# Optimization experiments

Hardware: AMD Instinct MI355X
Metric: run time of the kernel (lower is better)

## Reference

```python
import jax, jax.numpy as jnp
import numpy as np

B, N, E, H = 8, 16, 256, 256
EPS = 1e-5


def _ln(x, g, b):
    m = jnp.mean(x, axis=-1, keepdims=True)
    v = jnp.mean(jnp.square(x - m), axis=-1, keepdims=True)
    return (x - m) * jax.lax.rsqrt(v + EPS) * g + b


def setup_inputs() -> dict:
    key = jax.random.key(0)
    ks = jax.random.split(key, 24)
    s = 0.05
    inp = {
        "source_entities": jax.random.normal(ks[0], (B, N, E), jnp.float32),
        "source_relations": jax.random.uniform(ks[1], (B, N, N), jnp.float32),
        "target_entities": jax.random.normal(ks[2], (B, N, E), jnp.float32),
        "target_relations": jax.random.uniform(ks[3], (B, N, N), jnp.float32),
        # relation_encoder: Linear(2E->H), LayerNorm(H), ReLU, Linear(H->H)
        "rel_W1": jax.random.normal(ks[4], (2 * E, H), jnp.float32) * s,
        "rel_b1": jnp.zeros((H,), jnp.float32),
        "rel_g1": jnp.ones((H,), jnp.float32),
        "rel_be1": jnp.zeros((H,), jnp.float32),
        "rel_W2": jax.random.normal(ks[5], (H, H), jnp.float32) * s,
        "rel_b2": jnp.zeros((H,), jnp.float32),
        # mapping_network: Linear(2H->H), LayerNorm(H), ReLU, Linear(H->1)
        "map_W1": jax.random.normal(ks[6], (2 * H, H), jnp.float32) * s,
        "map_b1": jnp.zeros((H,), jnp.float32),
        "map_g": jnp.ones((H,), jnp.float32),
        "map_be": jnp.zeros((H,), jnp.float32),
        "map_W2": jax.random.normal(ks[7], (H, 1), jnp.float32) * s,
        "map_b2": jnp.zeros((1,), jnp.float32),
        # correspondence_scorer: Linear(2E->H), ReLU, Linear(H->1)
        "cor_W1": jax.random.normal(ks[8], (2 * E, H), jnp.float32) * s,
        "cor_b1": jnp.zeros((H,), jnp.float32),
        "cor_W2": jax.random.normal(ks[9], (H, 1), jnp.float32) * s,
        "cor_b2": jnp.zeros((1,), jnp.float32),
    }
    return inp


def _encode_relations(ent, rel, W1, b1, g1, be1, W2, b2):
    # ent: [B,N,E]; rel: [B,N,N].  Equivalent to cat([e_i, e_j]) @ W1 by
    # splitting W1 into the rows multiplying e_i and e_j (avoids concat).
    Wi, Wj = W1[:E], W1[E:]
    h = (jnp.einsum("bie,eh->bih", ent, Wi)[:, :, None, :]
         + jnp.einsum("bje,eh->bjh", ent, Wj)[:, None, :, :] + b1)  # [B,N,N,H]
    h = jax.nn.relu(_ln(h, g1, be1))
    h = jnp.einsum("bijh,hk->bijk", h, W2) + b2
    mask = (rel > 0).astype(h.dtype)[..., None]
    h = h * mask  # zeros where no relation, matching scatter into zeros tensor
    return h.reshape(ent.shape[0], N * N, H)


def _pairwise_score(a, b, W1, b1, W2, b2, g=None, be=None):
    # score over all (i,j) pairs: cat([a_i, b_j]) -> MLP -> scalar
    d = a.shape[-1]
    Wa, Wb = W1[:d], W1[d:]
    h = (jnp.einsum("bsd,dh->bsh", a, Wa)[:, :, None, :]
         + jnp.einsum("btd,dh->bth", b, Wb)[:, None, :, :] + b1)  # [B,S,T,H]
    if g is not None:
        h = _ln(h, g, be)
    h = jax.nn.relu(h)
    return (jnp.einsum("bsth,ho->bsto", h, W2) + b2)[..., 0]  # [B,S,T]


def reference(source_entities, source_relations, target_entities, target_relations,
              rel_W1, rel_b1, rel_g1, rel_be1, rel_W2, rel_b2,
              map_W1, map_b1, map_g, map_be, map_W2, map_b2,
              cor_W1, cor_b1, cor_W2, cor_b2):
    src_rel = _encode_relations(source_entities, source_relations,
                                rel_W1, rel_b1, rel_g1, rel_be1, rel_W2, rel_b2)
    tgt_rel = _encode_relations(target_entities, target_relations,
                                rel_W1, rel_b1, rel_g1, rel_be1, rel_W2, rel_b2)
    mapping_scores = _pairwise_score(src_rel, tgt_rel, map_W1, map_b1,
                                     map_W2, map_b2, map_g, map_be)
    corr_scores = _pairwise_score(source_entities, target_entities,
                                  cor_W1, cor_b1, cor_W2, cor_b2)
    mapping_scores = jax.nn.softmax(mapping_scores, axis=-1)
    corr_scores = jax.nn.softmax(corr_scores, axis=-1)
    return mapping_scores, corr_scores
```

## Files before the change

### kernel.cpp

```cpp
#include <hip/hip_runtime.h>

#define EDIM 256
#define HDIM 256

typedef float v2f __attribute__((ext_vector_type(2)));
__device__ __forceinline__ v2f splat2(float x) { v2f r; r.x = x; r.y = x; return r; }
__device__ __forceinline__ v2f mk2(float a, float b) { v2f r; r.x = a; r.y = b; return r; }
__device__ __forceinline__ v2f pkfma(v2f a, v2f b, v2f c) { return __builtin_elementwise_fma(a, b, c); }

__device__ __forceinline__ float waveAllSum(float v) {
  #pragma unroll
  for (int m = 32; m >= 1; m >>= 1) v += __shfl_xor(v, m, 64);
  return v;
}

__global__ __launch_bounds__(256) void k_proj(
    const float* __restrict__ srcE, const float* __restrict__ tgtE,
    const float* __restrict__ relW1, const float* __restrict__ relb1,
    const float* __restrict__ corW1, const float* __restrict__ corb1,
    const float* __restrict__ relW2, const float* __restrict__ relb2,
    const float* __restrict__ mapW1,
    float* __restrict__ Ps, float* __restrict__ Qs,
    float* __restrict__ Pt, float* __restrict__ Qt,
    float* __restrict__ CA, float* __restrict__ CB,
    float* __restrict__ Ca, float* __restrict__ Cb,
    float* __restrict__ da, float* __restrict__ db)
{
  const int which = blockIdx.x & 7;
  const int xb    = blockIdx.x >> 3;
  const int h     = threadIdx.x;
  if (which < 6 && xb >= 16) return;
  const int row0  = xb * 8;

  const float* A = nullptr; const float* W; const float* bias = nullptr;
  float* out;
  if (which == 0)      { A = srcE; W = relW1;              bias = relb1; out = Ps; }
  else if (which == 1) { A = srcE; W = relW1 + EDIM*HDIM;  out = Qs; }
  else if (which == 2) { A = tgtE; W = relW1;              bias = relb1; out = Pt; }
  else if (which == 3) { A = tgtE; W = relW1 + EDIM*HDIM;  out = Qt; }
  else if (which == 4) { A = srcE; W = corW1;              out = CA; }
  else if (which == 5) { A = tgtE; W = corW1 + EDIM*HDIM;  bias = corb1; out = CB; }
  else if (which == 6) { W = mapW1;                        out = Ca; }
  else                 { W = mapW1 + EDIM*HDIM;            out = Cb; }

  __shared__ float arow[8][EDIM];
  if (which < 6) {
    #pragma unroll
    for (int r = 0; r < 8; ++r) arow[r][h] = A[(row0 + r)*EDIM + h];
  } else if (xb < 32) {
    #pragma unroll
    for (int r = 0; r < 8; ++r) arow[r][h] = relW2[(row0 + r)*EDIM + h];
  } else {
    #pragma unroll
    for (int r = 0; r < 8; ++r) arow[r][h] = relb2[h];
  }
  __syncthreads();

  float acc[8];
  const float init = bias ? bias[h] : 0.0f;
  #pragma unroll
  for (int r = 0; r < 8; ++r) acc[r] = init;

  for (int d = 0; d < EDIM; d += 4) {
    const float w0 = W[(d+0)*HDIM + h];
    const float w1 = W[(d+1)*HDIM + h];
    const float w2 = W[(d+2)*HDIM + h];
    const float w3 = W[(d+3)*HDIM + h];
    #pragma unroll
    for (int r = 0; r < 8; ++r) {
      const float4 av = *(const float4*)&arow[r][d];
      acc[r] = fmaf(av.x,w0, fmaf(av.y,w1, fmaf(av.z,w2, fmaf(av.w,w3, acc[r]))));
    }
  }

  if (which < 6 || xb < 32) {
    #pragma unroll
    for (int r = 0; r < 8; ++r) out[(row0 + r)*HDIM + h] = acc[r];
  } else {
    float* d = (which == 6) ? da : db;
    d[h] = acc[0];
  }
}

__global__ __launch_bounds__(512) void k_encode(
    const float* __restrict__ Ps, const float* __restrict__ Qs,
    const float* __restrict__ relS,
    const float* __restrict__ Pt, const float* __restrict__ Qt,
    const float* __restrict__ relT,
    const float* __restrict__ g1, const float* __restrict__ be1,
    const float* __restrict__ Ca, const float* __restrict__ Cb,
    const float* __restrict__ da, const float* __restrict__ db,
    const float* __restrict__ mapb1,
    const float* __restrict__ mapg, const float* __restrict__ mapbe,
    const float* __restrict__ mapW2,
    float2* __restrict__ SAp, float* __restrict__ SAr, float* __restrict__ TB,
    float* __restrict__ rsS, float* __restrict__ qsS,
    float* __restrict__ rsT, float* __restrict__ qsT,
    float4* __restrict__ gbw)
{
  const int side = blockIdx.x & 1;
  const int bx   = blockIdx.x >> 1;
  const float* P   = side ? Pt   : Ps;
  const float* Q   = side ? Qt   : Qs;
  const float* rel = side ? relT : relS;

  const int row0 = bx * 8;
  const int b   = row0 >> 8;
  const int ij0 = row0 & 255;
  const int i   = ij0 >> 4;
  const int j0  = ij0 & 15;
  const int tid  = threadIdx.x;
  const int h    = tid & 255;
  const int rg   = tid >> 8;
  const int wave = tid >> 6;
  const int lane = tid & 63;

  if (side == 0 && bx == 0 && rg == 0)
    gbw[h] = make_float4(mapg[h], mapbe[h], mapW2[h], 0.0f);

  __shared__ v2f rlp[2][2][HDIM];
  __shared__ float red[8][8];

  const float pv = P[(b*16 + i)*HDIM + h];
  float x[4];
  #pragma unroll
  for (int r = 0; r < 4; ++r) x[r] = pv + Q[(b*16 + j0 + rg*4 + r)*HDIM + h];

  {
    float s1[4], s2[4];
    #pragma unroll
    for (int r = 0; r < 4; ++r) { s1[r] = x[r]; s2[r] = x[r]*x[r]; }
    #pragma unroll
    for (int m = 32; m >= 1; m >>= 1) {
      #pragma unroll
      for (int r = 0; r < 4; ++r) {
        s1[r] += __shfl_xor(s1[r], m, 64);
        s2[r] += __shfl_xor(s2[r], m, 64);
      }
    }
    if (lane == 0) {
      #pragma unroll
      for (int r = 0; r < 4; ++r) { red[wave][2*r] = s1[r]; red[wave][2*r+1] = s2[r]; }
    }
  }
  __syncthreads();

  {
    const float gh = g1[h], beh = be1[h];
    const int wb = rg*4;
    float val[4];
    #pragma unroll
    for (int r = 0; r < 4; ++r) {
      const float S1 = red[wb+0][2*r] + red[wb+1][2*r] + red[wb+2][2*r] + red[wb+3][2*r];
      const float S2 = red[wb+0][2*r+1] + red[wb+1][2*r+1] + red[wb+2][2*r+1] + red[wb+3][2*r+1];
      const float mean = S1 * (1.0f/256.0f);
      const float var  = S2 * (1.0f/256.0f) - mean*mean;
      const float rinv = rsqrtf(var + 1e-5f);
      val[r] = fmaxf(fmaf((x[r] - mean)*rinv, gh, beh), 0.0f);
    }
    rlp[rg][0][h] = mk2(val[0], val[1]);
    rlp[rg][1][h] = mk2(val[2], val[3]);
  }
  __syncthreads();

  const float* C = side ? Cb : Ca;
  v2f c01 = {0.f,0.f}, c23 = {0.f,0.f};
  #pragma unroll 2
  for (int k = 0; k < HDIM; k += 4) {
    const float w0 = C[(k+0)*HDIM + h];
    const float w1 = C[(k+1)*HDIM + h];
    const float w2 = C[(k+2)*HDIM + h];
    const float w3 = C[(k+3)*HDIM + h];
    const float4 pa = *(const float4*)&rlp[rg][0][k];
    const float4 pb = *(const float4*)&rlp[rg][0][k+2];
    const float4 qa = *(const float4*)&rlp[rg][1][k];
    const float4 qb = *(const float4*)&rlp[rg][1][k+2];
    c01 = pkfma(mk2(pa.x,pa.y), splat2(w0), c01);
    c01 = pkfma(mk2(pa.z,pa.w), splat2(w1), c01);
    c01 = pkfma(mk2(pb.x,pb.y), splat2(w2), c01);
    c01 = pkfma(mk2(pb.z,pb.w), splat2(w3), c01);
    c23 = pkfma(mk2(qa.x,qa.y), splat2(w0), c23);
    c23 = pkfma(mk2(qa.z,qa.w), splat2(w1), c23);
    c23 = pkfma(mk2(qb.x,qb.y), splat2(w2), c23);
    c23 = pkfma(mk2(qb.z,qb.w), splat2(w3), c23);
  }

  {
    const float dv = (side ? db : da)[h];
    c01 = c01 + splat2(dv);
    c23 = c23 + splat2(dv);
    const float* relRow = rel + (b*16 + i)*16;
    const int jb = j0 + rg*4;
    const v2f m01 = mk2(relRow[jb+0] > 0.f ? 1.f : 0.f, relRow[jb+1] > 0.f ? 1.f : 0.f);
    const v2f m23 = mk2(relRow[jb+2] > 0.f ? 1.f : 0.f, relRow[jb+3] > 0.f ? 1.f : 0.f);
    c01 = c01 * m01;
    c23 = c23 * m23;
    if (side) {
      const float mb = mapb1[h];
      c01 = c01 + splat2(mb);
      c23 = c23 + splat2(mb);
    }
  }

  {
    float s1[4] = {c01.x, c01.y, c23.x, c23.y};
    float s2[4] = {c01.x*c01.x, c01.y*c01.y, c23.x*c23.x, c23.y*c23.y};
    #pragma unroll
    for (int m = 32; m >= 1; m >>= 1) {
      #pragma unroll
      for (int r = 0; r < 4; ++r) {
        s1[r] += __shfl_xor(s1[r], m, 64);
        s2[r] += __shfl_xor(s2[r], m, 64);
      }
    }
    __syncthreads();
    if (lane == 0) {
      #pragma unroll
      for (int r = 0; r < 4; ++r) { red[wave][2*r] = s1[r]; red[wave][2*r+1] = s2[r]; }
    }
  }
  __syncthreads();
  if (tid < 16) {
    const int rg2 = tid >> 3, idx = tid & 7, r = idx >> 1;
    const int wb = rg2*4;
    const float v = red[wb+0][idx] + red[wb+1][idx] + red[wb+2][idx] + red[wb+3][idx];
    float* rs = side ? rsT : rsS;
    float* qs = side ? qsT : qsS;
    const int row = row0 + rg2*4 + r;
    if (idx & 1) qs[row] = v; else rs[row] = v;
  }

  const int rbase = row0 + rg*4;
  if (side == 0) {
    const int spBase = b*128 + ((ij0 + rg*4) >> 1);
    SAp[(spBase + 0)*HDIM + h] = make_float2(c01.x, c01.y);
    SAp[(spBase + 1)*HDIM + h] = make_float2(c23.x, c23.y);
    SAr[(rbase + 0)*HDIM + h] = c01.x;
    SAr[(rbase + 1)*HDIM + h] = c01.y;
    SAr[(rbase + 2)*HDIM + h] = c23.x;
    SAr[(rbase + 3)*HDIM + h] = c23.y;
  } else {
    TB[(rbase + 0)*HDIM + h] = c01.x;
    TB[(rbase + 1)*HDIM + h] = c01.y;
    TB[(rbase + 2)*HDIM + h] = c23.x;
    TB[(rbase + 3)*HDIM + h] = c23.y;
  }
}

__global__ __launch_bounds__(256) void k_cross(
    const float* __restrict__ SAr, const float* __restrict__ TB,
    float* __restrict__ G)
{
  const int b    = blockIdx.x & 7;
  const int rest = blockIdx.x >> 3;
  const int s0 = (rest & 7) * 32;
  const int t0 = (rest >> 3) * 32;
  const int tx = threadIdx.x & 15;
  const int ty = threadIdx.x >> 4;

  const float* SAb = SAr + ((b<<8) + s0)*HDIM;
  const float* TBb = TB  + ((b<<8) + t0)*HDIM;

  __shared__ float As[32][68], Bs[32][68];
  float acc00 = 0.f, acc01 = 0.f, acc10 = 0.f, acc11 = 0.f;

  const int lr = threadIdx.x >> 3;
  const int lc = (threadIdx.x & 7) * 8;

  for (int kk = 0; kk < HDIM; kk += 64) {
    *(float4*)&As[lr][lc]   = *(const float4*)&SAb[lr*HDIM + kk + lc];
    *(float4*)&As[lr][lc+4] = *(const float4*)&SAb[lr*HDIM + kk + lc + 4];
    *(float4*)&Bs[lr][lc]   = *(const float4*)&TBb[lr*HDIM + kk + lc];
    *(float4*)&Bs[lr][lc+4] = *(const float4*)&TBb[lr*HDIM + kk + lc + 4];
    __syncthreads();
    #pragma unroll
    for (int k = 0; k < 64; k += 4) {
      const float4 a0 = *(const float4*)&As[tx][k];
      const float4 a1 = *(const float4*)&As[tx+16][k];
      const float4 b0 = *(const float4*)&Bs[ty][k];
      const float4 b1 = *(const float4*)&Bs[ty+16][k];
      acc00 = fmaf(a0.x,b0.x, fmaf(a0.y,b0.y, fmaf(a0.z,b0.z, fmaf(a0.w,b0.w, acc00))));
      acc01 = fmaf(a0.x,b1.x, fmaf(a0.y,b1.y, fmaf(a0.z,b1.z, fmaf(a0.w,b1.w, acc01))));
      acc10 = fmaf(a1.x,b0.x, fmaf(a1.y,b0.y, fmaf(a1.z,b0.z, fmaf(a1.w,b0.w, acc10))));
      acc11 = fmaf(a1.x,b1.x, fmaf(a1.y,b1.y, fmaf(a1.z,b1.z, fmaf(a1.w,b1.w, acc11))));
    }
    __syncthreads();
  }

  float* Gb = G + (((b<<8) + t0)<<8) + s0;
  Gb[(ty   )*256 + tx     ] = acc00;
  Gb[(ty   )*256 + tx + 16] = acc10;
  Gb[(ty+16)*256 + tx     ] = acc01;
  Gb[(ty+16)*256 + tx + 16] = acc11;
}

__global__ __launch_bounds__(256) void k_scores(
    const float2* __restrict__ SApf, const float* __restrict__ TB,
    const float* __restrict__ G,
    const float* __restrict__ rsS, const float* __restrict__ qsS,
    const float* __restrict__ rsT, const float* __restrict__ qsT,
    const float4* __restrict__ gbw,
    const float* __restrict__ CA, const float* __restrict__ CB,
    const float* __restrict__ cW2,
    float* __restrict__ mapOut, float* __restrict__ corOut)
{
  const int wave = threadIdx.x >> 6;
  const int lane = threadIdx.x & 63;

  if (blockIdx.x >= 512) {
    const int bs = (blockIdx.x - 512)*4 + wave;
    const int b  = bs >> 4;
    const float4 ca4 = *(const float4*)(CA + bs*HDIM + lane*4);
    const float4 w24 = *(const float4*)(cW2 + lane*4);
    float sc[16];
    #pragma unroll
    for (int t = 0; t < 16; ++t) {
      const float4 cb4 = *(const float4*)(CB + (b*16 + t)*HDIM + lane*4);
      float p = fmaxf(ca4.x + cb4.x, 0.0f)*w24.x
              + fmaxf(ca4.y + cb4.y, 0.0f)*w24.y
              + fmaxf(ca4.z + cb4.z, 0.0f)*w24.z
              + fmaxf(ca4.w + cb4.w, 0.0f)*w24.w;
      sc[t] = waveAllSum(p);
    }
    float mx = sc[0];
    #pragma unroll
    for (int t = 1; t < 16; ++t) mx = fmaxf(mx, sc[t]);
    float se = 0.0f;
    #pragma unroll
    for (int t = 0; t < 16; ++t) { sc[t] = __expf(sc[t] - mx); se += sc[t]; }
    if (lane < 16) corOut[bs*16 + lane] = sc[lane] / se;
    return;
  }

  const int b  = blockIdx.x & 7;
  const int s0 = (blockIdx.x >> 3) * 4;
  const int t  = (wave << 6) + lane;

  const float* tbrow = TB + ((b<<8) + t)*HDIM;
  const v2f* sp0 = (const v2f*)SApf + ((b<<7) + (s0>>1))*HDIM;
  const v2f* sp1 = sp0 + HDIM;

  v2f al01, bt01, al23, bt23;
  {
    const float4 gv = *(const float4*)&G[(((b<<8) + t)<<8) + s0];
    const float rt = rsT[(b<<8) + t];
    const float qt = qsT[(b<<8) + t];
    const float Gv[4] = {gv.x, gv.y, gv.z, gv.w};
    float alv[4], btv[4];
    #pragma unroll
    for (int si = 0; si < 4; ++si) {
      const float mean = (rsS[(b<<8) + s0 + si] + rt) * (1.0f/256.0f);
      const float e2   = (qsS[(b<<8) + s0 + si] + qt + 2.0f*Gv[si]) * (1.0f/256.0f);
      const float rinv = rsqrtf(e2 - mean*mean + 1e-5f);
      alv[si] = rinv;
      btv[si] = -mean * rinv;
    }
    al01 = mk2(alv[0], alv[1]); bt01 = mk2(btv[0], btv[1]);
    al23 = mk2(alv[2], alv[3]); bt23 = mk2(btv[2], btv[3]);
  }

  v2f acc01 = {0.f,0.f}, acc23 = {0.f,0.f};
  const v2f zero = {0.f,0.f};
  #pragma unroll 2
  for (int h = 0; h < HDIM; h += 4) {
    const float4 tb4 = *(const float4*)&tbrow[h];
    const v2f a0 = sp0[h], a1 = sp0[h+1], a2 = sp0[h+2], a3 = sp0[h+3];
    const v2f c0 = sp1[h], c1 = sp1[h+1], c2 = sp1[h+2], c3 = sp1[h+3];
    const float4 q0 = gbw[h], q1 = gbw[h+1], q2 = gbw[h+2], q3 = gbw[h+3];
    v2f u, r;
    u = pkfma(a0 + splat2(tb4.x), al01, bt01);
    r = __builtin_elementwise_max(pkfma(u, splat2(q0.x), splat2(q0.y)), zero);
    acc01 = pkfma(r, splat2(q0.z), acc01);
    u = pkfma(c0 + splat2(tb4.x), al23, bt23);
    r = __builtin_elementwise_max(pkfma(u, splat2(q0.x), splat2(q0.y)), zero);
    acc23 = pkfma(r, splat2(q0.z), acc23);

    u = pkfma(a1 + splat2(tb4.y), al01, bt01);
    r = __builtin_elementwise_max(pkfma(u, splat2(q1.x), splat2(q1.y)), zero);
    acc01 = pkfma(r, splat2(q1.z), acc01);
    u = pkfma(c1 + splat2(tb4.y), al23, bt23);
    r = __builtin_elementwise_max(pkfma(u, splat2(q1.x), splat2(q1.y)), zero);
    acc23 = pkfma(r, splat2(q1.z), acc23);

    u = pkfma(a2 + splat2(tb4.z), al01, bt01);
    r = __builtin_elementwise_max(pkfma(u, splat2(q2.x), splat2(q2.y)), zero);
    acc01 = pkfma(r, splat2(q2.z), acc01);
    u = pkfma(c2 + splat2(tb4.z), al23, bt23);
    r = __builtin_elementwise_max(pkfma(u, splat2(q2.x), splat2(q2.y)), zero);
    acc23 = pkfma(r, splat2(q2.z), acc23);

    u = pkfma(a3 + splat2(tb4.w), al01, bt01);
    r = __builtin_elementwise_max(pkfma(u, splat2(q3.x), splat2(q3.y)), zero);
    acc01 = pkfma(r, splat2(q3.z), acc01);
    u = pkfma(c3 + splat2(tb4.w), al23, bt23);
    r = __builtin_elementwise_max(pkfma(u, splat2(q3.x), splat2(q3.y)), zero);
    acc23 = pkfma(r, splat2(q3.z), acc23);
  }

  __shared__ float sc[4][256];
  sc[0][t] = acc01.x; sc[1][t] = acc01.y; sc[2][t] = acc23.x; sc[3][t] = acc23.y;
  __syncthreads();

  float v0 = sc[wave][lane];
  float v1 = sc[wave][lane + 64];
  float v2 = sc[wave][lane + 128];
  float v3 = sc[wave][lane + 192];
  float mx = fmaxf(fmaxf(v0, v1), fmaxf(v2, v3));
  #pragma unroll
  for (int m = 32; m >= 1; m >>= 1) mx = fmaxf(mx, __shfl_xor(mx, m, 64));
  const float e0 = __expf(v0 - mx), e1 = __expf(v1 - mx);
  const float e2 = __expf(v2 - mx), e3 = __expf(v3 - mx);
  const float se = waveAllSum(e0 + e1 + e2 + e3);
  const float inv = 1.0f / se;
  float* orow = mapOut + ((b<<8) + s0 + wave)*256;
  orow[lane]       = e0 * inv;
  orow[lane + 64]  = e1 * inv;
  orow[lane + 128] = e2 * inv;
  orow[lane + 192] = e3 * inv;
}

extern "C" void kernel_launch(void* const* d_in, const int* in_sizes, int n_in,
                              void* d_out, int out_size, void* d_ws, size_t ws_size,
                              hipStream_t stream) {
  const float* srcE  = (const float*)d_in[0];
  const float* srcR  = (const float*)d_in[1];
  const float* tgtE  = (const float*)d_in[2];
  const float* tgtR  = (const float*)d_in[3];
  const float* relW1 = (const float*)d_in[4];
  const float* relb1 = (const float*)d_in[5];
  const float* relg1 = (const float*)d_in[6];
  const float* relbe1= (const float*)d_in[7];
  const float* relW2 = (const float*)d_in[8];
  const float* relb2 = (const float*)d_in[9];
  const float* mapW1 = (const float*)d_in[10];
  const float* mapb1 = (const float*)d_in[11];
  const float* mapg  = (const float*)d_in[12];
  const float* mapbe = (const float*)d_in[13];
  const float* mapW2 = (const float*)d_in[14];
  const float* corW1 = (const float*)d_in[16];
  const float* corb1 = (const float*)d_in[17];
  const float* corW2 = (const float*)d_in[18];

  float* ws   = (float*)d_ws;
  float* Ps   = ws;
  float* Qs   = Ps   + 32768;
  float* Pt   = Qs   + 32768;
  float* Qt   = Pt   + 32768;
  float* CA   = Qt   + 32768;
  float* CB   = CA   + 32768;
  float2* SAp = (float2*)(CB + 32768);
  float* SAr  = (float*)(SAp + 262144);
  float* TB   = SAr + 524288;
  float* G    = TB  + 524288;
  float* rsS  = G + 524288;
  float* qsS  = rsS + 2048;
  float* rsT  = qsS + 2048;
  float* qsT  = rsT + 2048;
  float4* gbw = (float4*)(qsT + 2048);
  float* Ca   = (float*)gbw + 1024;
  float* Cb   = Ca + 65536;
  float* da   = Cb + 65536;
  float* db   = da + 256;

  float* mapOut = (float*)d_out;
  float* corOut = mapOut + 524288;

  k_proj<<<264, 256, 0, stream>>>(srcE, tgtE, relW1, relb1, corW1, corb1,
                                  relW2, relb2, mapW1,
                                  Ps, Qs, Pt, Qt, CA, CB,
                                  Ca, Cb, da, db);
  k_encode<<<512, 512, 0, stream>>>(Ps, Qs, srcR,
                                    Pt, Qt, tgtR,
                                    relg1, relbe1,
                                    Ca, Cb, da, db,
                                    mapb1, mapg, mapbe, mapW2,
                                    SAp, SAr, TB, rsS, qsS, rsT, qsT, gbw);
  k_cross<<<512, 256, 0, stream>>>(SAr, TB, G);
  k_scores<<<544, 256, 0, stream>>>(SAp, TB, G, rsS, qsS, rsT, qsT, gbw,
                                    CA, CB, corW2, mapOut, corOut);
}
```

Baseline: 68.60 us.

## Split k_scores hidden dim across waves and compute eight source rows per block

```diff
diff --git a/kernel.cpp b/kernel.cpp
--- a/kernel.cpp
+++ b/kernel.cpp
@@ -294,7 +294,7 @@
   Gb[(ty+16)*256 + tx + 16] = acc11;
 }
 
-__global__ __launch_bounds__(256) void k_scores(
+__global__ __launch_bounds__(1024) void k_scores(
     const float2* __restrict__ SApf, const float* __restrict__ TB,
     const float* __restrict__ G,
     const float* __restrict__ rsS, const float* __restrict__ qsS,
@@ -307,8 +307,8 @@
   const int wave = threadIdx.x >> 6;
   const int lane = threadIdx.x & 63;
 
-  if (blockIdx.x >= 512) {
-    const int bs = (blockIdx.x - 512)*4 + wave;
+  if (blockIdx.x >= 256) {
+    const int bs = (blockIdx.x - 256)*16 + wave;
     const int b  = bs >> 4;
     const float4 ca4 = *(const float4*)(CA + bs*HDIM + lane*4);
     const float4 w24 = *(const float4*)(cW2 + lane*4);
@@ -333,90 +333,101 @@
   }
 
   const int b  = blockIdx.x & 7;
-  const int s0 = (blockIdx.x >> 3) * 4;
-  const int t  = (wave << 6) + lane;
+  const int s0 = (blockIdx.x >> 3) * 8;
+  const int tq = wave & 3;
+  const int hq = wave >> 2;
+  const int t  = (tq << 6) + lane;
+  const int h0 = __builtin_amdgcn_readfirstlane(hq * 64);
 
   const float* tbrow = TB + ((b<<8) + t)*HDIM;
-  const v2f* sp0 = (const v2f*)SApf + ((b<<7) + (s0>>1))*HDIM;
-  const v2f* sp1 = sp0 + HDIM;
-
-  v2f al01, bt01, al23, bt23;
+  const v2f* sp[4];
+  #pragma unroll
+  for (int p = 0; p < 4; ++p)
+    sp[p] = (const v2f*)SApf + ((b<<7) + (s0>>1) + p)*HDIM;
+
+  v2f al[4], bt[4];
   {
-    const float4 gv = *(const float4*)&G[(((b<<8) + t)<<8) + s0];
+    const float4 gv0 = *(const float4*)&G[(((b<<8) + t)<<8) + s0];
+    const float4 gv1 = *(const float4*)&G[(((b<<8) + t)<<8) + s0 + 4];
     const float rt = rsT[(b<<8) + t];
     const float qt = qsT[(b<<8) + t];
-    const float Gv[4] = {gv.x, gv.y, gv.z, gv.w};
-    float alv[4], btv[4];
-    #pragma unroll
-    for (int si = 0; si < 4; ++si) {
+    const float Gv[8] = {gv0.x, gv0.y, gv0.z, gv0.w, gv1.x, gv1.y, gv1.z, gv1.w};
+    float alv[8], btv[8];
+    #pragma unroll
+    for (int si = 0; si < 8; ++si) {
       const float mean = (rsS[(b<<8) + s0 + si] + rt) * (1.0f/256.0f);
       const float e2   = (qsS[(b<<8) + s0 + si] + qt + 2.0f*Gv[si]) * (1.0f/256.0f);
       const float rinv = rsqrtf(e2 - mean*mean + 1e-5f);
       alv[si] = rinv;
       btv[si] = -mean * rinv;
     }
-    al01 = mk2(alv[0], alv[1]); bt01 = mk2(btv[0], btv[1]);
-    al23 = mk2(alv[2], alv[3]); bt23 = mk2(btv[2], btv[3]);
-  }
-
-  v2f acc01 = {0.f,0.f}, acc23 = {0.f,0.f};
+    #pragma unroll
+    for (int p = 0; p < 4; ++p) {
+      al[p] = mk2(alv[2*p], alv[2*p+1]);
+      bt[p] = mk2(btv[2*p], btv[2*p+1]);
+    }
+  }
+
+  v2f acc[4] = {{0.f,0.f},{0.f,0.f},{0.f,0.f},{0.f,0.f}};
   const v2f zero = {0.f,0.f};
   #pragma unroll 2
-  for (int h = 0; h < HDIM; h += 4) {
+  for (int h = h0; h < h0 + 64; h += 4) {
     const float4 tb4 = *(const float4*)&tbrow[h];
-    const v2f a0 = sp0[h], a1 = sp0[h+1], a2 = sp0[h+2], a3 = sp0[h+3];
-    const v2f c0 = sp1[h], c1 = sp1[h+1], c2 = sp1[h+2], c3 = sp1[h+3];
     const float4 q0 = gbw[h], q1 = gbw[h+1], q2 = gbw[h+2], q3 = gbw[h+3];
-    v2f u, r;
-    u = pkfma(a0 + splat2(tb4.x), al01, bt01);
-    r = __builtin_elementwise_max(pkfma(u, splat2(q0.x), splat2(q0.y)), zero);
-    acc01 = pkfma(r, splat2(q0.z), acc01);
-    u = pkfma(c0 + splat2(tb4.x), al23, bt23);
-    r = __builtin_elementwise_max(pkfma(u, splat2(q0.x), splat2(q0.y)), zero);
-    acc23 = pkfma(r, splat2(q0.z), acc23);
-
-    u = pkfma(a1 + splat2(tb4.y), al01, bt01);
-    r = __builtin_elementwise_max(pkfma(u, splat2(q1.x), splat2(q1.y)), zero);
-    acc01 = pkfma(r, splat2(q1.z), acc01);
-    u = pkfma(c1 + splat2(tb4.y), al23, bt23);
-    r = __builtin_elementwise_max(pkfma(u, splat2(q1.x), splat2(q1.y)), zero);
-    acc23 = pkfma(r, splat2(q1.z), acc23);
-
-    u = pkfma(a2 + splat2(tb4.z), al01, bt01);
-    r = __builtin_elementwise_max(pkfma(u, splat2(q2.x), splat2(q2.y)), zero);
-    acc01 = pkfma(r, splat2(q2.z), acc01);
-    u = pkfma(c2 + splat2(tb4.z), al23, bt23);
-    r = __builtin_elementwise_max(pkfma(u, splat2(q2.x), splat2(q2.y)), zero);
-    acc23 = pkfma(r, splat2(q2.z), acc23);
-
-    u = pkfma(a3 + splat2(tb4.w), al01, bt01);
-    r = __builtin_elementwise_max(pkfma(u, splat2(q3.x), splat2(q3.y)), zero);
-    acc01 = pkfma(r, splat2(q3.z), acc01);
-    u = pkfma(c3 + splat2(tb4.w), al23, bt23);
-    r = __builtin_elementwise_max(pkfma(u, splat2(q3.x), splat2(q3.y)), zero);
-    acc23 = pkfma(r, splat2(q3.z), acc23);
-  }
-
-  __shared__ float sc[4][256];
-  sc[0][t] = acc01.x; sc[1][t] = acc01.y; sc[2][t] = acc23.x; sc[3][t] = acc23.y;
-  __syncthreads();
-
-  float v0 = sc[wave][lane];
-  float v1 = sc[wave][lane + 64];
-  float v2 = sc[wave][lane + 128];
-  float v3 = sc[wave][lane + 192];
-  float mx = fmaxf(fmaxf(v0, v1), fmaxf(v2, v3));
+    #pragma unroll
+    for (int p = 0; p < 4; ++p) {
+      const v2f a0 = sp[p][h], a1 = sp[p][h+1], a2 = sp[p][h+2], a3 = sp[p][h+3];
+      v2f u, r;
+      u = pkfma(a0 + splat2(tb4.x), al[p], bt[p]);
+      r = __builtin_elementwise_max(pkfma(u, splat2(q0.x), splat2(q0.y)), zero);
+      acc[p] = pkfma(r, splat2(q0.z), acc[p]);
+      u = pkfma(a1 + splat2(tb4.y), al[p], bt[p]);
+      r = __builtin_elementwise_max(pkfma(u, splat2(q1.x), splat2(q1.y)), zero);
+      acc[p] = pkfma(r, splat2(q1.z), acc[p]);
+      u = pkfma(a2 + splat2(tb4.z), al[p], bt[p]);
+      r = __builtin_elementwise_max(pkfma(u, splat2(q2.x), splat2(q2.y)), zero);
+      acc[p] = pkfma(r, splat2(q2.z), acc[p]);
+      u = pkfma(a3 + splat2(tb4.w), al[p], bt[p]);
+      r = __builtin_elementwise_max(pkfma(u, splat2(q3.x), splat2(q3.y)), zero);
+      acc[p] = pkfma(r, splat2(q3.z), acc[p]);
+    }
+  }
+
+  __shared__ float pg[4][4][8][64];
   #pragma unroll
-  for (int m = 32; m >= 1; m >>= 1) mx = fmaxf(mx, __shfl_xor(mx, m, 64));
-  const float e0 = __expf(v0 - mx), e1 = __expf(v1 - mx);
-  const float e2 = __expf(v2 - mx), e3 = __expf(v3 - mx);
-  const float se = waveAllSum(e0 + e1 + e2 + e3);
-  const float inv = 1.0f / se;
-  float* orow = mapOut + ((b<<8) + s0 + wave)*256;
-  orow[lane]       = e0 * inv;
-  orow[lane + 64]  = e1 * inv;
-  orow[lane + 128] = e2 * inv;
-  orow[lane + 192] = e3 * inv;
+  for (int p = 0; p < 4; ++p) {
+    pg[hq][tq][2*p  ][lane] = acc[p].x;
+    pg[hq][tq][2*p+1][lane] = acc[p].y;
+  }
+  __syncthreads();
+
+  __shared__ float sc[8][256];
+  if (hq == 0) {
+    #pragma unroll
+    for (int si = 0; si < 8; ++si)
+      sc[si][t] = pg[0][tq][si][lane] + pg[1][tq][si][lane]
+                + pg[2][tq][si][lane] + pg[3][tq][si][lane];
+  }
+  __syncthreads();
+
+  if (wave < 8) {
+    float v0 = sc[wave][lane];
+    float v1 = sc[wave][lane + 64];
+    float v2 = sc[wave][lane + 128];
+    float v3 = sc[wave][lane + 192];
+    float mx = fmaxf(fmaxf(v0, v1), fmaxf(v2, v3));
+    #pragma unroll
+    for (int m = 32; m >= 1; m >>= 1) mx = fmaxf(mx, __shfl_xor(mx, m, 64));
+    const float e0 = __expf(v0 - mx), e1 = __expf(v1 - mx);
+    const float e2 = __expf(v2 - mx), e3 = __expf(v3 - mx);
+    const float se = waveAllSum(e0 + e1 + e2 + e3);
+    const float inv = 1.0f / se;
+    float* orow = mapOut + ((b<<8) + s0 + wave)*256;
+    orow[lane]       = e0 * inv;
+    orow[lane + 64]  = e1 * inv;
+    orow[lane + 128] = e2 * inv;
+    orow[lane + 192] = e3 * inv;
+  }
 }
 
 extern "C" void kernel_launch(void* const* d_in, const int* in_sizes, int n_in,
@@ -476,6 +487,6 @@
                                     mapb1, mapg, mapbe, mapW2,
                                     SAp, SAr, TB, rsS, qsS, rsT, qsT, gbw);
   k_cross<<<512, 256, 0, stream>>>(SAr, TB, G);
-  k_scores<<<544, 256, 0, stream>>>(SAp, TB, G, rsS, qsS, rsT, qsT, gbw,
-                                    CA, CB, corW2, mapOut, corOut);
-}
+  k_scores<<<264, 1024, 0, stream>>>(SAp, TB, G, rsS, qsS, rsT, qsT, gbw,
+                                     CA, CB, corW2, mapOut, corOut);
+}
```

Result: slower. 70.00 us (+2.1%).
